# Kernel optimization log

Measured on AMD Instinct MI355X. Metric: run time of the kernel, lower is better.

## Reference

```python
import jax, jax.numpy as jnp
import numpy as np

B, T, D, H, K, V, W = 2, 2048, 768, 12, 64, 64, 1024
EPS = 1e-6


def setup_inputs() -> dict:
    key = jax.random.key(0)
    ks = jax.random.split(key, 10)
    std = 0.02
    return {
        "x": jax.random.normal(ks[0], (B, T, D), jnp.float32),
        "gdn_state": jax.random.normal(ks[1], (B, H, K, V), jnp.float32),
        "Wq": jax.random.normal(ks[2], (D, H * K), jnp.float32) * std,
        "Wk": jax.random.normal(ks[3], (D, H * K), jnp.float32) * std,
        "Wv": jax.random.normal(ks[4], (D, H * K), jnp.float32) * std,
        "Wo": jax.random.normal(ks[5], (H * K, D), jnp.float32) * std,
        "Wgq": jax.random.normal(ks[6], (D, H * K), jnp.float32) * std,
        "Wro": jax.random.normal(ks[7], (H * V, D), jnp.float32) * std,
        "Wg": jax.random.normal(ks[8], (D, H), jnp.float32) * std,
        "bg": jnp.full((H,), 1.0, jnp.float32),  # swa_gate_init
        "norm_w": jnp.ones((D,), jnp.float32),
    }


def reference(x, gdn_state, Wq, Wk, Wv, Wo, Wgq, Wro, Wg, bg, norm_w):
    # RMSNorm
    xn = x * jax.lax.rsqrt(jnp.mean(x * x, axis=-1, keepdims=True) + EPS) * norm_w

    def proj(w):  # (B,T,D)@(D,HK) -> (B,H,T,K)
        return (xn @ w).reshape(B, T, H, K).transpose(0, 2, 1, 3)

    q, k, v = proj(Wq), proj(Wk), proj(Wv)
    scale = K ** -0.5

    scores = jnp.einsum("bhqk,bhsk->bhqs", q, k) * scale  # (B,H,T,T)
    i = jnp.arange(T)[:, None]
    j = jnp.arange(T)[None, :]
    allowed = (j <= i) & (j >= i - W)  # causal sliding window
    scores = jnp.where(allowed, scores, -jnp.inf)
    attn = jax.nn.softmax(scores, axis=-1)

    local = jnp.einsum("bhqs,bhsk->bhqk", attn, v)
    local = local.transpose(0, 2, 1, 3).reshape(B, T, H * K) @ Wo  # (B,T,D)

    # GDN state retrieval
    qg = jax.nn.relu((xn @ Wgq).reshape(B, T, H, K).transpose(0, 2, 1, 3))  # (B,H,T,K)
    retrieved = jnp.einsum("bhkv,bhtk->bhtv", gdn_state, qg)  # (B,H,T,V)
    retrieval = retrieved.transpose(0, 2, 1, 3).reshape(B, T, H * V) @ Wro  # (B,T,D)
    gate = jax.nn.sigmoid(xn @ Wg + bg)  # (B,T,H)
    retrieval = jnp.mean(gate, axis=-1, keepdims=True) * retrieval

    return x + local + retrieval
```

## Files before the change

### kernel.cpp

```cpp
#include <hip/hip_runtime.h>
#include <math.h>
#include <stdint.h>

typedef float f32x4 __attribute__((ext_vector_type(4)));
typedef __bf16 bf16x8 __attribute__((ext_vector_type(8)));
typedef __bf16 bf16x4 __attribute__((ext_vector_type(4)));

constexpr int Bc = 2, Tc = 2048, Dc = 768, Hc = 12, Wc = 1024;
#define CEXP 0.18033688011112042f

__device__ __forceinline__ f32x4 mfma_bf16(bf16x8 a, bf16x8 b, f32x4 c) {
    return __builtin_amdgcn_mfma_f32_16x16x32_bf16(a, b, c, 0, 0, 0);
}
__device__ __forceinline__ void gload16(const void* g, void* l) {
    __builtin_amdgcn_global_load_lds(
        (const __attribute__((address_space(1))) uint32_t*)g,
        (__attribute__((address_space(3))) uint32_t*)l, 16, 0, 0);
}
__device__ __forceinline__ uint32_t pack2(float a, float b) {
    union { __bf16 h[2]; uint32_t u; } x;
    x.h[0] = (__bf16)a; x.h[1] = (__bf16)b; return x.u;
}
__device__ __forceinline__ void s_wait_vm4() { asm volatile("s_waitcnt vmcnt(4)" ::: "memory"); }
__device__ __forceinline__ void s_wait_vm2() { asm volatile("s_waitcnt vmcnt(2)" ::: "memory"); }
__device__ __forceinline__ void s_wait_vm0() { asm volatile("s_waitcnt vmcnt(0)" ::: "memory"); }
__device__ __forceinline__ void s_wait_lgkm0() { asm volatile("s_waitcnt lgkmcnt(0)" ::: "memory"); }
__device__ __forceinline__ void bar()        { __builtin_amdgcn_s_barrier(); }
__device__ __forceinline__ void wait_tiles2(int infl) {
    if (infl >= 2) s_wait_vm4();
    else if (infl == 1) s_wait_vm2();
    else s_wait_vm0();
}

__global__ __launch_bounds__(256) void k_prep_w(
    const float* __restrict__ Wq, const float* __restrict__ Wk,
    const float* __restrict__ Wv, const float* __restrict__ Wgq,
    const float* __restrict__ Wo, const float* __restrict__ Wro,
    __bf16* __restrict__ wTproj, __bf16* __restrict__ wTout)
{
    __shared__ __bf16 ldsT[64][66];
    const int wsel = blockIdx.y;
    const float* srcs[6] = {Wq, Wk, Wv, Wgq, Wo, Wro};
    const float* src = srcs[wsel];
    __bf16* dst; int dstride, koff;
    if (wsel < 4) { dst = wTproj + (size_t)wsel * Dc * Dc; dstride = Dc;  koff = 0; }
    else if (wsel == 4) { dst = wTout; dstride = 1536; koff = 0; }
    else { dst = wTout; dstride = 1536; koff = 768; }
    const float scale = (wsel == 0) ? CEXP : 1.0f;

    int tile = blockIdx.x;
    int tk = tile % 12, tn = tile / 12;
    int k0 = tk * 64, n0 = tn * 64;
    int i = threadIdx.x, rsub = i >> 4, c4 = i & 15;
#pragma unroll
    for (int rep = 0; rep < 4; ++rep) {
        int row = rep * 16 + rsub;
        float4 v = *(const float4*)(src + (size_t)(k0 + row) * Dc + n0 + c4 * 4);
        ldsT[c4 * 4 + 0][row] = (__bf16)(v.x * scale);
        ldsT[c4 * 4 + 1][row] = (__bf16)(v.y * scale);
        ldsT[c4 * 4 + 2][row] = (__bf16)(v.z * scale);
        ldsT[c4 * 4 + 3][row] = (__bf16)(v.w * scale);
    }
    __syncthreads();
#pragma unroll
    for (int rep = 0; rep < 4; ++rep) {
        int n = rep * 16 + rsub;
        bf16x4 o = *(const bf16x4*)&ldsT[n][c4 * 4];
        *(bf16x4*)(dst + (size_t)(n0 + n) * dstride + koff + k0 + c4 * 4) = o;
    }
}

__global__ __launch_bounds__(256) void k_prep_state(
    const float* __restrict__ st, __bf16* __restrict__ stT)
{
    int idx = blockIdx.x * 256 + threadIdx.x;
    int bh = idx >> 12, kk = (idx >> 6) & 63, vv = idx & 63;
    stT[(size_t)bh * 4096 + vv * 64 + kk] = (__bf16)st[idx];
}

__global__ __launch_bounds__(256) void k_prep_wgt(
    const float* __restrict__ Wg, float* __restrict__ WgT)
{
    int i = blockIdx.x * 256 + threadIdx.x;
    int h = i / Dc, d = i - h * Dc;
    WgT[i] = Wg[d * 12 + h];
}

__global__ __launch_bounds__(256) void k_rmsnorm(
    const float* __restrict__ x, const float* __restrict__ norm_w,
    __bf16* __restrict__ xnb)
{
    int row = blockIdx.x, tid = threadIdx.x;
    const float* xr = x + (size_t)row * Dc;
    float4 v = make_float4(0.f, 0.f, 0.f, 0.f);
    float ss = 0.f;
    if (tid < 192) {
        v = ((const float4*)xr)[tid];
        ss = v.x * v.x + v.y * v.y + v.z * v.z + v.w * v.w;
    }
#pragma unroll
    for (int m = 32; m; m >>= 1) ss += __shfl_xor(ss, m, 64);
    __shared__ float red[4];
    if ((tid & 63) == 0) red[tid >> 6] = ss;
    __syncthreads();
    float tot = red[0] + red[1] + red[2] + red[3];
    float rms = rsqrtf(tot * (1.f / 768.f) + 1e-6f);
    if (tid < 192) {
        float4 nw = ((const float4*)norm_w)[tid];
        bf16x4 o;
        o[0] = (__bf16)(v.x * rms * nw.x);
        o[1] = (__bf16)(v.y * rms * nw.y);
        o[2] = (__bf16)(v.z * rms * nw.z);
        o[3] = (__bf16)(v.w * rms * nw.w);
        *(bf16x4*)(xnb + (size_t)row * Dc + tid * 4) = o;
    }
}

__global__ __launch_bounds__(256) void k_gate(
    const __bf16* __restrict__ xnb, const float* __restrict__ WgT,
    const float* __restrict__ bg, float* __restrict__ gmean)
{
    int row = blockIdx.x * 4 + (threadIdx.x >> 6);
    int lane = threadIdx.x & 63;
    const __bf16* xr = xnb + (size_t)row * Dc;
    float p[12];
#pragma unroll
    for (int h = 0; h < 12; ++h) p[h] = 0.f;
    for (int d = lane; d < Dc; d += 64) {
        float xv = (float)xr[d];
#pragma unroll
        for (int h = 0; h < 12; ++h) p[h] += xv * WgT[h * Dc + d];
    }
#pragma unroll
    for (int h = 0; h < 12; ++h) {
#pragma unroll
        for (int m = 32; m; m >>= 1) p[h] += __shfl_xor(p[h], m, 64);
    }
    if (lane == 0) {
        float s = 0.f;
#pragma unroll
        for (int h = 0; h < 12; ++h) s += 1.f / (1.f + expf(-(p[h] + bg[h])));
        gmean[row] = s * (1.f / 12.f);
    }
}

template <int MODE>
__global__ __launch_bounds__(512, 6) void k_gemm(
    const __bf16* __restrict__ A, const __bf16* __restrict__ BT,
    const float* __restrict__ xres, float* __restrict__ outf,
    __bf16* __restrict__ qb, __bf16* __restrict__ kbf,
    __bf16* __restrict__ vtb, __bf16* __restrict__ qgb)
{
    constexpr int BM = (MODE == 0) ? 128 : 64;
    constexpr int BN = (MODE == 0) ? 128 : 64;
    constexpr int KD = (MODE == 0) ? 768 : 1536;
    constexpr int BK = (MODE == 0) ? 32 : 64;
    constexpr int KI = BK / 32;
    constexpr int MI = (MODE == 0) ? 4 : 1;
    constexpr int NI = 2;
    constexpr int MT = 4096 / BM;
    constexpr int NK = KD / BK;
    constexpr int GR = BK / 8;
    __shared__ __bf16 As[2][BM * BK];
    __shared__ __bf16 Bs[2][BN * BK];
    const int tid = threadIdx.x, w = tid >> 6, lane = tid & 63;
    const int g = lane >> 4, t = lane & 15;
    int id = blockIdx.x, xcd = id & 7, l = id >> 3;
    int nid = xcd * 96 + l;
    int m0 = (nid % MT) * BM, n0 = (nid / MT) * BN;
    const __bf16* Abase = A + (size_t)m0 * KD;
    const __bf16* Bbase = BT + (size_t)n0 * KD;
    const int wrow = (MODE == 0) ? (w >> 2) * 64 : (w >> 1) * 16;
    const int wcol = (MODE == 0) ? (w & 3) * 32 : (w & 1) * 32;

    auto STAGE = [&](int buf, int k0) {
        int row = tid / GR, cix = tid % GR;
        gload16(Abase + (size_t)row * KD + k0 + cix * 8, &As[buf][tid * 8]);
        gload16(Bbase + (size_t)row * KD + k0 + cix * 8, &Bs[buf][tid * 8]);
    };

    f32x4 acc[MI][NI] = {};
    STAGE(0, 0);
    STAGE(1, BK);
    for (int ks = 0; ks < NK; ++ks) {
        if (ks == NK - 1) s_wait_vm0(); else s_wait_vm2();
        bar();
        const __bf16* Ab = As[ks & 1];
        const __bf16* Bb = Bs[ks & 1];
        bf16x8 af[MI][KI], bfr[NI][KI];
#pragma unroll
        for (int kk = 0; kk < KI; ++kk) {
#pragma unroll
            for (int mi = 0; mi < MI; ++mi)
                af[mi][kk] = *(const bf16x8*)(Ab + (wrow + mi * 16 + t) * BK + kk * 32 + g * 8);
#pragma unroll
            for (int ni = 0; ni < NI; ++ni)
                bfr[ni][kk] = *(const bf16x8*)(Bb + (wcol + ni * 16 + t) * BK + kk * 32 + g * 8);
        }
        s_wait_lgkm0();
        __builtin_amdgcn_sched_barrier(0);
        bar();
        if (ks + 2 < NK) STAGE(ks & 1, (ks + 2) * BK);
        __builtin_amdgcn_s_setprio(1);
#pragma unroll
        for (int kk = 0; kk < KI; ++kk)
#pragma unroll
            for (int mi = 0; mi < MI; ++mi)
#pragma unroll
                for (int ni = 0; ni < NI; ++ni)
                    acc[mi][ni] = mfma_bf16(af[mi][kk], bfr[ni][kk], acc[mi][ni]);
        __builtin_amdgcn_s_setprio(0);
    }
    const int region = (MODE == 0) ? (n0 / 768) : 0;
#pragma unroll
    for (int mi = 0; mi < MI; ++mi)
#pragma unroll
        for (int ni = 0; ni < NI; ++ni)
#pragma unroll
            for (int r = 0; r < 4; ++r) {
                int grow = m0 + wrow + mi * 16 + g * 4 + r;
                int gcol = n0 + wcol + ni * 16 + t;
                float v = acc[mi][ni][r];
                if (MODE == 1) {
                    size_t idx = (size_t)grow * Dc + gcol;
                    outf[idx] = xres[idx] + v;
                } else {
                    int c = gcol - region * 768;
                    int h = c >> 6, kd = c & 63;
                    int b = grow >> 11, ti = grow & (Tc - 1);
                    if (region == 0)
                        qb[((size_t)(b * Hc + h) * Tc + ti) * 64 + kd] = (__bf16)v;
                    else if (region == 1) {
                        int kds = kd ^ ((ti & 7) << 3);
                        kbf[((size_t)(b * Hc + h) * Tc + ti) * 64 + kds] = (__bf16)v;
                    } else if (region == 2) {
                        int kap = ti & 63;
                        int rho = (kap & 32) | (((kap >> 2) & 3) << 3) |
                                  (((kap >> 4) & 1) << 2) | (kap & 3);
                        int ts = (ti & ~63) | (rho ^ ((kd & 7) << 3));
                        vtb[((size_t)(b * Hc + h) * 64 + kd) * Tc + ts] = (__bf16)v;
                    } else
                        qgb[((size_t)(b * Hc + h) * Tc + ti) * 64 + kd] = (__bf16)fmaxf(v, 0.f);
                }
            }
}

__global__ __launch_bounds__(512, 6) void k_attn(
    const __bf16* __restrict__ q, const __bf16* __restrict__ k,
    const __bf16* __restrict__ vt, const __bf16* __restrict__ qg,
    const __bf16* __restrict__ stateT, const float* __restrict__ gmean,
    __bf16* __restrict__ ac)
{
    __shared__ __bf16 Ks[3][64 * 64];
    __shared__ __bf16 Vs[3][64 * 64];
    int id = blockIdx.x, xcd = id & 7, l = id >> 3;
    int nid = xcd * 96 + l;
    int sblk = nid & 31, h = (nid >> 5) % Hc, b = nid / (32 * Hc);
    int tid = threadIdx.x;
    int w = tid >> 6, lane = tid & 63;
    int g = lane >> 4, t = lane & 15;
    int q0 = sblk * 64, qw = q0 + (w & 3) * 16;
    const int myPar = w >> 2;
    const __bf16* qb = q + (size_t)(b * Hc + h) * Tc * 64;
    const __bf16* kb = k + (size_t)(b * Hc + h) * Tc * 64;
    const __bf16* vb = vt + (size_t)(b * Hc + h) * 64 * Tc;

    bf16x8 qf0 = *(const bf16x8*)(qb + (size_t)(qw + t) * 64 + g * 8);
    bf16x8 qf1 = *(const bf16x8*)(qb + (size_t)(qw + t) * 64 + 32 + g * 8);

    const int qi = qw + t;
    const int lowB = qi - Wc;
    const int xr = t & 7;

    f32x4 oacc[4] = {};
    float lsum = 0.f;

    const int s_begin = (q0 >= Wc) ? q0 - Wc : 0;
    const int NT = (q0 + 64 - s_begin) >> 6;

    auto STAGE = [&](int buf, int s0) {
        int ch = tid;
        gload16(kb + (size_t)(s0 + (ch >> 3)) * 64 + (ch & 7) * 8, &Ks[buf][ch * 8]);
        gload16(vb + (size_t)(ch >> 3) * Tc + s0 + (ch & 7) * 8, &Vs[buf][ch * 8]);
    };

    STAGE(0, s_begin);
    if (NT > 1) STAGE(1, s_begin + 64);
    if (NT > 2) STAGE(2, s_begin + 128);
    int buf = 0;
    for (int it = 0; it < NT; ++it) {
        int s0 = s_begin + it * 64;
        wait_tiles2(NT - 1 - it);
        bar();
        if ((it & 1) == myPar) {
            const __bf16* Kt = Ks[buf];
            const __bf16* Vt = Vs[buf];
            f32x4 sc[4];
            __builtin_amdgcn_s_setprio(1);
#pragma unroll
            for (int sub = 0; sub < 4; ++sub) {
                const __bf16* kr = Kt + (sub * 16 + t) * 64;
                bf16x8 kA = *(const bf16x8*)(kr + ((g ^ xr) << 3));
                bf16x8 kB = *(const bf16x8*)(kr + (((g + 4) ^ xr) << 3));
                f32x4 s = {};
                s = mfma_bf16(kA, qf0, s);
                s = mfma_bf16(kB, qf1, s);
                sc[sub] = s;
            }
            __builtin_amdgcn_s_setprio(0);
            float pv[4][4];
#pragma unroll
            for (int sub = 0; sub < 4; ++sub)
#pragma unroll
                for (int r = 0; r < 4; ++r) {
                    int kk = s0 + sub * 16 + g * 4 + r;
                    float e = exp2f(sc[sub][r]);
                    float val = (kk <= qi && kk >= lowB) ? e : 0.f;
                    pv[sub][r] = val;
                    lsum += val;
                }
            __builtin_amdgcn_s_setprio(1);
#pragma unroll
            for (int ks = 0; ks < 2; ++ks) {
                union { uint32_t u[4]; bf16x8 v; } pf;
                pf.u[0] = pack2(pv[ks * 2][0], pv[ks * 2][1]);
                pf.u[1] = pack2(pv[ks * 2][2], pv[ks * 2][3]);
                pf.u[2] = pack2(pv[ks * 2 + 1][0], pv[ks * 2 + 1][1]);
                pf.u[3] = pack2(pv[ks * 2 + 1][2], pv[ks * 2 + 1][3]);
#pragma unroll
                for (int n = 0; n < 4; ++n) {
                    const __bf16* vrow = Vt + (n * 16 + t) * 64;
                    bf16x8 vf = *(const bf16x8*)(vrow + ((((ks * 4) + g) ^ xr) << 3));
                    oacc[n] = mfma_bf16(pf.v, vf, oacc[n]);
                }
            }
            __builtin_amdgcn_s_setprio(0);
        }
        s_wait_lgkm0();
        __builtin_amdgcn_sched_barrier(0);
        bar();
        if (it + 3 < NT) STAGE(buf, s0 + 192);
        buf = (buf == 2) ? 0 : buf + 1;
    }
    float* cb = (float*)&Ks[0][0];
    if (w >= 4) {
        float* dst = cb + ((size_t)((w - 4) * 64 + lane)) * 20;
#pragma unroll
        for (int n = 0; n < 4; ++n) *(f32x4*)(dst + n * 4) = oacc[n];
        dst[16] = lsum;
    }
    bar();
    if (w < 4) {
        const float* src = cb + ((size_t)(w * 64 + lane)) * 20;
#pragma unroll
        for (int n = 0; n < 4; ++n) oacc[n] += *(const f32x4*)(src + n * 4);
        lsum += src[16];
        lsum += __shfl_xor(lsum, 16, 64);
        lsum += __shfl_xor(lsum, 32, 64);
        float linv = 1.f / lsum;
        float lq[4];
#pragma unroll
        for (int r = 0; r < 4; ++r) lq[r] = __shfl(linv, g * 4 + r, 64);
#pragma unroll
        for (int n = 0; n < 4; ++n)
#pragma unroll
            for (int r = 0; r < 4; ++r) {
                int qrow = qw + g * 4 + r;
                ac[(size_t)(b * Tc + qrow) * 1536 + h * 64 + n * 16 + t] =
                    (__bf16)(oacc[n][r] * lq[r]);
            }
        const __bf16* qgp = qg + (size_t)(b * Hc + h) * Tc * 64;
        const __bf16* sb = stateT + (size_t)(b * Hc + h) * 4096;
        bf16x8 a0 = *(const bf16x8*)(qgp + (size_t)(qw + t) * 64 + g * 8);
        bf16x8 a1 = *(const bf16x8*)(qgp + (size_t)(qw + t) * 64 + 32 + g * 8);
#pragma unroll
        for (int n = 0; n < 4; ++n) {
            bf16x8 b0 = *(const bf16x8*)(sb + (n * 16 + t) * 64 + g * 8);
            bf16x8 b1 = *(const bf16x8*)(sb + (n * 16 + t) * 64 + 32 + g * 8);
            f32x4 acc2 = {};
            acc2 = mfma_bf16(a0, b0, acc2);
            acc2 = mfma_bf16(a1, b1, acc2);
#pragma unroll
            for (int r = 0; r < 4; ++r) {
                int ti = qw + g * 4 + r;
                float gm = gmean[b * Tc + ti];
                ac[(size_t)(b * Tc + ti) * 1536 + 768 + h * 64 + n * 16 + t] =
                    (__bf16)(acc2[r] * gm);
            }
        }
    }
}

extern "C" void kernel_launch(void* const* d_in, const int* in_sizes, int n_in,
                              void* d_out, int out_size, void* d_ws, size_t ws_size,
                              hipStream_t stream) {
    (void)in_sizes; (void)n_in; (void)out_size; (void)ws_size;
    const float* x     = (const float*)d_in[0];
    const float* gdn   = (const float*)d_in[1];
    const float* Wq    = (const float*)d_in[2];
    const float* Wk    = (const float*)d_in[3];
    const float* Wv    = (const float*)d_in[4];
    const float* Wo    = (const float*)d_in[5];
    const float* Wgq   = (const float*)d_in[6];
    const float* Wro   = (const float*)d_in[7];
    const float* Wg    = (const float*)d_in[8];
    const float* bg    = (const float*)d_in[9];
    const float* normw = (const float*)d_in[10];
    float* out = (float*)d_out;

    char* p = (char*)d_ws;
    auto alloc = [&](size_t bytes) -> char* {
        char* r = p; p += (bytes + 255) & ~(size_t)255; return r;
    };
    constexpr size_t NROW = (size_t)Bc * Tc;
    __bf16* xnb    = (__bf16*)alloc(NROW * Dc * 2);
    __bf16* wTproj = (__bf16*)alloc((size_t)4 * Dc * Dc * 2);
    __bf16* wTout  = (__bf16*)alloc((size_t)Dc * 1536 * 2);
    __bf16* stT    = (__bf16*)alloc((size_t)Bc * Hc * 64 * 64 * 2);
    __bf16* qbuf   = (__bf16*)alloc(NROW * Dc * 2);
    __bf16* kbuf   = (__bf16*)alloc(NROW * Dc * 2);
    __bf16* qgbuf  = (__bf16*)alloc(NROW * Dc * 2);
    __bf16* vtbuf  = (__bf16*)alloc(NROW * Dc * 2);
    __bf16* ac     = (__bf16*)alloc(NROW * 1536 * 2);
    float*  gmean  = (float*)alloc(NROW * 4);
    float*  WgT    = (float*)alloc((size_t)12 * Dc * 4);

    k_prep_w<<<dim3(144, 6), 256, 0, stream>>>(Wq, Wk, Wv, Wgq, Wo, Wro, wTproj, wTout);
    k_prep_state<<<(Bc * Hc * 64 * 64) / 256, 256, 0, stream>>>(gdn, stT);
    k_prep_wgt<<<36, 256, 0, stream>>>(Wg, WgT);
    k_rmsnorm<<<NROW, 256, 0, stream>>>(x, normw, xnb);
    k_gate<<<NROW / 4, 256, 0, stream>>>(xnb, WgT, bg, gmean);

    k_gemm<0><<<768, 512, 0, stream>>>(xnb, wTproj, nullptr, nullptr,
                                       qbuf, kbuf, vtbuf, qgbuf);
    k_attn<<<768, 512, 0, stream>>>(qbuf, kbuf, vtbuf, qgbuf, stT, gmean, ac);
    k_gemm<1><<<768, 512, 0, stream>>>(ac, wTout, x, out,
                                       nullptr, nullptr, nullptr, nullptr);
}
```

Measured before the change: 140.5 us.

## Enlarge GEMM tiles and give each attention wave its own query rows

Both GEMMs move to larger output tiles (256x256 for the projection, 128x128 for the output) with BK fixed at 32. This cuts the block count to 192 and increases per-wave MFMA work and operand reuse. The attention kernel now gives each of the 8 waves its own 16 query rows over a 128-row block, instead of splitting key tiles across two wave groups and merging partial results through LDS, which removes the merge barrier. In exchange there are fewer blocks than the 256 CUs, more registers per thread (launch bounds lowered to 2), and less parallelism in attention.

```diff
diff --git a/kernel.cpp b/kernel.cpp
--- a/kernel.cpp
+++ b/kernel.cpp
@@ -145,73 +145,77 @@
 }
 
 template <int MODE>
-__global__ __launch_bounds__(512, 6) void k_gemm(
+__global__ __launch_bounds__(512, 2) void k_gemm(
     const __bf16* __restrict__ A, const __bf16* __restrict__ BT,
     const float* __restrict__ xres, float* __restrict__ outf,
     __bf16* __restrict__ qb, __bf16* __restrict__ kbf,
     __bf16* __restrict__ vtb, __bf16* __restrict__ qgb)
 {
-    constexpr int BM = (MODE == 0) ? 128 : 64;
-    constexpr int BN = (MODE == 0) ? 128 : 64;
+    constexpr int BM = (MODE == 0) ? 256 : 128;
+    constexpr int BN = (MODE == 0) ? 256 : 128;
     constexpr int KD = (MODE == 0) ? 768 : 1536;
-    constexpr int BK = (MODE == 0) ? 32 : 64;
-    constexpr int KI = BK / 32;
-    constexpr int MI = (MODE == 0) ? 4 : 1;
-    constexpr int NI = 2;
+    constexpr int BK = 32;
+    constexpr int MI = (MODE == 0) ? 8 : 4;
+    constexpr int NI = (MODE == 0) ? 4 : 2;
     constexpr int MT = 4096 / BM;
     constexpr int NK = KD / BK;
     constexpr int GR = BK / 8;
+    constexpr int CHA = BM * GR / 512;
+    constexpr int CHB = BN * GR / 512;
     __shared__ __bf16 As[2][BM * BK];
     __shared__ __bf16 Bs[2][BN * BK];
     const int tid = threadIdx.x, w = tid >> 6, lane = tid & 63;
     const int g = lane >> 4, t = lane & 15;
     int id = blockIdx.x, xcd = id & 7, l = id >> 3;
-    int nid = xcd * 96 + l;
+    int nid = xcd * 24 + l;
     int m0 = (nid % MT) * BM, n0 = (nid / MT) * BN;
     const __bf16* Abase = A + (size_t)m0 * KD;
     const __bf16* Bbase = BT + (size_t)n0 * KD;
-    const int wrow = (MODE == 0) ? (w >> 2) * 64 : (w >> 1) * 16;
-    const int wcol = (MODE == 0) ? (w & 3) * 32 : (w & 1) * 32;
+    const int wrow = (MODE == 0) ? (w >> 2) * 128 : (w >> 2) * 64;
+    const int wcol = (MODE == 0) ? (w & 3) * 64 : (w & 3) * 32;
 
     auto STAGE = [&](int buf, int k0) {
-        int row = tid / GR, cix = tid % GR;
-        gload16(Abase + (size_t)row * KD + k0 + cix * 8, &As[buf][tid * 8]);
-        gload16(Bbase + (size_t)row * KD + k0 + cix * 8, &Bs[buf][tid * 8]);
+#pragma unroll
+        for (int c = 0; c < CHA; ++c) {
+            int chunk = c * 512 + tid, row = chunk / GR, cix = chunk % GR;
+            gload16(Abase + (size_t)row * KD + k0 + cix * 8, &As[buf][chunk * 8]);
+        }
+#pragma unroll
+        for (int c = 0; c < CHB; ++c) {
+            int chunk = c * 512 + tid, row = chunk / GR, cix = chunk % GR;
+            gload16(Bbase + (size_t)row * KD + k0 + cix * 8, &Bs[buf][chunk * 8]);
+        }
     };
 
     f32x4 acc[MI][NI] = {};
     STAGE(0, 0);
     STAGE(1, BK);
     for (int ks = 0; ks < NK; ++ks) {
-        if (ks == NK - 1) s_wait_vm0(); else s_wait_vm2();
+        if (ks == NK - 1) s_wait_vm0();
+        else if (CHA + CHB == 4) s_wait_vm4();
+        else s_wait_vm2();
         bar();
         const __bf16* Ab = As[ks & 1];
         const __bf16* Bb = Bs[ks & 1];
-        bf16x8 af[MI][KI], bfr[NI][KI];
-#pragma unroll
-        for (int kk = 0; kk < KI; ++kk) {
-#pragma unroll
-            for (int mi = 0; mi < MI; ++mi)
-                af[mi][kk] = *(const bf16x8*)(Ab + (wrow + mi * 16 + t) * BK + kk * 32 + g * 8);
-#pragma unroll
-            for (int ni = 0; ni < NI; ++ni)
-                bfr[ni][kk] = *(const bf16x8*)(Bb + (wcol + ni * 16 + t) * BK + kk * 32 + g * 8);
-        }
+        bf16x8 af[MI], bfr[NI];
+#pragma unroll
+        for (int mi = 0; mi < MI; ++mi)
+            af[mi] = *(const bf16x8*)(Ab + (wrow + mi * 16 + t) * BK + g * 8);
+#pragma unroll
+        for (int ni = 0; ni < NI; ++ni)
+            bfr[ni] = *(const bf16x8*)(Bb + (wcol + ni * 16 + t) * BK + g * 8);
         s_wait_lgkm0();
         __builtin_amdgcn_sched_barrier(0);
         bar();
         if (ks + 2 < NK) STAGE(ks & 1, (ks + 2) * BK);
         __builtin_amdgcn_s_setprio(1);
 #pragma unroll
-        for (int kk = 0; kk < KI; ++kk)
-#pragma unroll
-            for (int mi = 0; mi < MI; ++mi)
-#pragma unroll
-                for (int ni = 0; ni < NI; ++ni)
-                    acc[mi][ni] = mfma_bf16(af[mi][kk], bfr[ni][kk], acc[mi][ni]);
+        for (int mi = 0; mi < MI; ++mi)
+#pragma unroll
+            for (int ni = 0; ni < NI; ++ni)
+                acc[mi][ni] = mfma_bf16(af[mi], bfr[ni], acc[mi][ni]);
         __builtin_amdgcn_s_setprio(0);
     }
-    const int region = (MODE == 0) ? (n0 / 768) : 0;
 #pragma unroll
     for (int mi = 0; mi < MI; ++mi)
 #pragma unroll
@@ -225,6 +229,7 @@
                     size_t idx = (size_t)grow * Dc + gcol;
                     outf[idx] = xres[idx] + v;
                 } else {
+                    int region = (gcol >= 2304) ? 3 : (gcol >= 1536) ? 2 : (gcol >= 768) ? 1 : 0;
                     int c = gcol - region * 768;
                     int h = c >> 6, kd = c & 63;
                     int b = grow >> 11, ti = grow & (Tc - 1);
@@ -254,13 +259,12 @@
     __shared__ __bf16 Ks[3][64 * 64];
     __shared__ __bf16 Vs[3][64 * 64];
     int id = blockIdx.x, xcd = id & 7, l = id >> 3;
-    int nid = xcd * 96 + l;
-    int sblk = nid & 31, h = (nid >> 5) % Hc, b = nid / (32 * Hc);
+    int nid = xcd * 48 + l;
+    int sblk = nid & 15, h = (nid >> 4) % Hc, b = nid / (16 * Hc);
     int tid = threadIdx.x;
     int w = tid >> 6, lane = tid & 63;
     int g = lane >> 4, t = lane & 15;
-    int q0 = sblk * 64, qw = q0 + (w & 3) * 16;
-    const int myPar = w >> 2;
+    int q0 = sblk * 128, qw = q0 + w * 16;
     const __bf16* qb = q + (size_t)(b * Hc + h) * Tc * 64;
     const __bf16* kb = k + (size_t)(b * Hc + h) * Tc * 64;
     const __bf16* vb = vt + (size_t)(b * Hc + h) * 64 * Tc;
@@ -276,7 +280,7 @@
     float lsum = 0.f;
 
     const int s_begin = (q0 >= Wc) ? q0 - Wc : 0;
-    const int NT = (q0 + 64 - s_begin) >> 6;
+    const int NT = (q0 + 128 - s_begin) >> 6;
 
     auto STAGE = [&](int buf, int s0) {
         int ch = tid;
@@ -292,7 +296,7 @@
         int s0 = s_begin + it * 64;
         wait_tiles2(NT - 1 - it);
         bar();
-        if ((it & 1) == myPar) {
+        {
             const __bf16* Kt = Ks[buf];
             const __bf16* Vt = Vs[buf];
             f32x4 sc[4];
@@ -342,51 +346,37 @@
         if (it + 3 < NT) STAGE(buf, s0 + 192);
         buf = (buf == 2) ? 0 : buf + 1;
     }
-    float* cb = (float*)&Ks[0][0];
-    if (w >= 4) {
-        float* dst = cb + ((size_t)((w - 4) * 64 + lane)) * 20;
-#pragma unroll
-        for (int n = 0; n < 4; ++n) *(f32x4*)(dst + n * 4) = oacc[n];
-        dst[16] = lsum;
-    }
-    bar();
-    if (w < 4) {
-        const float* src = cb + ((size_t)(w * 64 + lane)) * 20;
-#pragma unroll
-        for (int n = 0; n < 4; ++n) oacc[n] += *(const f32x4*)(src + n * 4);
-        lsum += src[16];
-        lsum += __shfl_xor(lsum, 16, 64);
-        lsum += __shfl_xor(lsum, 32, 64);
-        float linv = 1.f / lsum;
-        float lq[4];
-#pragma unroll
-        for (int r = 0; r < 4; ++r) lq[r] = __shfl(linv, g * 4 + r, 64);
-#pragma unroll
-        for (int n = 0; n < 4; ++n)
-#pragma unroll
-            for (int r = 0; r < 4; ++r) {
-                int qrow = qw + g * 4 + r;
-                ac[(size_t)(b * Tc + qrow) * 1536 + h * 64 + n * 16 + t] =
-                    (__bf16)(oacc[n][r] * lq[r]);
-            }
-        const __bf16* qgp = qg + (size_t)(b * Hc + h) * Tc * 64;
-        const __bf16* sb = stateT + (size_t)(b * Hc + h) * 4096;
-        bf16x8 a0 = *(const bf16x8*)(qgp + (size_t)(qw + t) * 64 + g * 8);
-        bf16x8 a1 = *(const bf16x8*)(qgp + (size_t)(qw + t) * 64 + 32 + g * 8);
-#pragma unroll
-        for (int n = 0; n < 4; ++n) {
-            bf16x8 b0 = *(const bf16x8*)(sb + (n * 16 + t) * 64 + g * 8);
-            bf16x8 b1 = *(const bf16x8*)(sb + (n * 16 + t) * 64 + 32 + g * 8);
-            f32x4 acc2 = {};
-            acc2 = mfma_bf16(a0, b0, acc2);
-            acc2 = mfma_bf16(a1, b1, acc2);
-#pragma unroll
-            for (int r = 0; r < 4; ++r) {
-                int ti = qw + g * 4 + r;
-                float gm = gmean[b * Tc + ti];
-                ac[(size_t)(b * Tc + ti) * 1536 + 768 + h * 64 + n * 16 + t] =
-                    (__bf16)(acc2[r] * gm);
-            }
+    lsum += __shfl_xor(lsum, 16, 64);
+    lsum += __shfl_xor(lsum, 32, 64);
+    float linv = 1.f / lsum;
+    float lq[4];
+#pragma unroll
+    for (int r = 0; r < 4; ++r) lq[r] = __shfl(linv, g * 4 + r, 64);
+#pragma unroll
+    for (int n = 0; n < 4; ++n)
+#pragma unroll
+        for (int r = 0; r < 4; ++r) {
+            int qrow = qw + g * 4 + r;
+            ac[(size_t)(b * Tc + qrow) * 1536 + h * 64 + n * 16 + t] =
+                (__bf16)(oacc[n][r] * lq[r]);
+        }
+    const __bf16* qgp = qg + (size_t)(b * Hc + h) * Tc * 64;
+    const __bf16* sb = stateT + (size_t)(b * Hc + h) * 4096;
+    bf16x8 a0 = *(const bf16x8*)(qgp + (size_t)(qw + t) * 64 + g * 8);
+    bf16x8 a1 = *(const bf16x8*)(qgp + (size_t)(qw + t) * 64 + 32 + g * 8);
+#pragma unroll
+    for (int n = 0; n < 4; ++n) {
+        bf16x8 b0 = *(const bf16x8*)(sb + (n * 16 + t) * 64 + g * 8);
+        bf16x8 b1 = *(const bf16x8*)(sb + (n * 16 + t) * 64 + 32 + g * 8);
+        f32x4 acc2 = {};
+        acc2 = mfma_bf16(a0, b0, acc2);
+        acc2 = mfma_bf16(a1, b1, acc2);
+#pragma unroll
+        for (int r = 0; r < 4; ++r) {
+            int ti = qw + g * 4 + r;
+            float gm = gmean[b * Tc + ti];
+            ac[(size_t)(b * Tc + ti) * 1536 + 768 + h * 64 + n * 16 + t] =
+                (__bf16)(acc2[r] * gm);
         }
     }
 }
@@ -431,9 +421,9 @@
     k_rmsnorm<<<NROW, 256, 0, stream>>>(x, normw, xnb);
     k_gate<<<NROW / 4, 256, 0, stream>>>(xnb, WgT, bg, gmean);
 
-    k_gemm<0><<<768, 512, 0, stream>>>(xnb, wTproj, nullptr, nullptr,
+    k_gemm<0><<<192, 512, 0, stream>>>(xnb, wTproj, nullptr, nullptr,
                                        qbuf, kbuf, vtbuf, qgbuf);
-    k_attn<<<768, 512, 0, stream>>>(qbuf, kbuf, vtbuf, qgbuf, stT, gmean, ac);
-    k_gemm<1><<<768, 512, 0, stream>>>(ac, wTout, x, out,
+    k_attn<<<384, 512, 0, stream>>>(qbuf, kbuf, vtbuf, qgbuf, stT, gmean, ac);
+    k_gemm<1><<<192, 512, 0, stream>>>(ac, wTout, x, out,
                                        nullptr, nullptr, nullptr, nullptr);
 }
```

After: 151.0 us. 7.5% more time.
